# Kernel optimization log

Measured on AMD Instinct MI355X. Metric: run time of the kernel, lower is better.

## Reference

```python
import jax, jax.numpy as jnp
import numpy as np

MB, SEQ, EMBDIM, N_TOKENS = 8, 2048, 64, 8192


def setup_inputs() -> dict:
    key = jax.random.key(0)
    k1, k2 = jax.random.split(key)
    X = jax.random.normal(k1, (MB, SEQ, EMBDIM), dtype=jnp.float32)
    weight = jax.random.normal(k2, (N_TOKENS, EMBDIM), dtype=jnp.float32)
    return {"X": X, "weight": weight}


def reference(X, weight):
    adotb = jnp.einsum("bse,ne->bsn", X, weight)            # [mb, seq, n_tokens]
    adota = jnp.sum(X * X, axis=-1, keepdims=True)           # [mb, seq, 1]
    bdotb = jnp.sum(weight * weight, axis=-1)                # [n_tokens]
    dist = adota - 2.0 * adotb + bdotb                       # [mb, seq, n_tokens]
    return jnp.argmin(dist, axis=-1)                         # [mb, seq] int indices
```

## Files before the change

kernel.cpp:

```cpp
#include <hip/hip_runtime.h>
#include <math.h>

#define EMB     64
#define NTOK    8192
#define NQ      16384
#define TPB     256
#define CSPLIT  4
#define CRANGE  (NTOK / CSPLIT)
#define BQ      128
#define TILE_C  128
#define NT      (CRANGE / TILE_C)
#define TCH     (TILE_C * EMB)
#define NXBLK   (NQ / BQ)

typedef _Float16 half8 __attribute__((ext_vector_type(8)));
typedef float    f32x4 __attribute__((ext_vector_type(4)));

__device__ __forceinline__ void gl2lds16(const _Float16* g, _Float16* l) {
    __builtin_amdgcn_global_load_lds(
        (const __attribute__((address_space(1))) unsigned int*)g,
        (__attribute__((address_space(3))) unsigned int*)l, 16, 0, 0);
}

__device__ __forceinline__ unsigned long long pack_di(float d, int idx) {
    unsigned int u = __float_as_uint(d);
    unsigned int m = (u & 0x80000000u) ? ~u : (u | 0x80000000u);
    return ((unsigned long long)m << 32) | (unsigned int)idx;
}

__global__ void prep_kernel(const float* __restrict__ W,
                            _Float16* __restrict__ Wh, _Float16* __restrict__ Wl,
                            float* __restrict__ ynorm,
                            unsigned long long* __restrict__ packed,
                            int* __restrict__ cnt) {
    const int gtid = blockIdx.x * blockDim.x + threadIdx.x;
    if (gtid < NQ)    packed[gtid] = ~0ull;
    if (gtid < NXBLK) cnt[gtid] = 0;
    if (gtid < NTOK * 8) {
        const int u  = gtid;
        const int g  = u >> 7, rem = u & 127;
        const int kb = rem >> 6, ln = rem & 63;
        const int r  = ln & 15, lq = ln >> 4;
        const int c  = g * 16 + r;
        const float* wp = W + (size_t)c * EMB + kb * 32 + lq * 8;
        float4 v0 = *(const float4*)wp;
        float4 v1 = *(const float4*)(wp + 4);
        float xv[8] = {v0.x, v0.y, v0.z, v0.w, v1.x, v1.y, v1.z, v1.w};
        half8 h, l;
#pragma unroll
        for (int j = 0; j < 8; ++j) {
            _Float16 hh = (_Float16)xv[j];
            h[j] = hh;
            l[j] = (_Float16)(xv[j] - (float)hh);
        }
        *(half8*)(Wh + (size_t)u * 8) = h;
        *(half8*)(Wl + (size_t)u * 8) = l;
    } else if (gtid < NTOK * 8 + NTOK) {
        const int c = gtid - NTOK * 8;
        const float4* w4 = (const float4*)(W + (size_t)c * EMB);
        float s = 0.f;
#pragma unroll
        for (int i = 0; i < EMB / 4; ++i) {
            float4 v = w4[i];
            s = fmaf(v.x, v.x, s); s = fmaf(v.y, v.y, s);
            s = fmaf(v.z, v.z, s); s = fmaf(v.w, v.w, s);
        }
        ynorm[c] = s;
    }
}

__global__ __launch_bounds__(TPB, 2) void vq_mfma_kernel(
    const float* __restrict__ X,
    const _Float16* __restrict__ Wh, const _Float16* __restrict__ Wl,
    const float* __restrict__ ynorm,
    unsigned long long* __restrict__ packed,
    int* __restrict__ cnt, int* __restrict__ out)
{
    __shared__ __align__(16) _Float16 LdsH[3][TCH];
    __shared__ __align__(16) float    Lyn[CRANGE];
    __shared__ float RedV[2][BQ];
    __shared__ int   RedI[2][BQ];
    __shared__ int   fin;

    const int t    = threadIdx.x;
    const int lane = t & 63;
    const int wid  = t >> 6;
    const int wq   = wid & 1;
    const int wy   = wid >> 1;
    const int l15  = lane & 15;
    const int lq   = lane >> 4;

    const int bx     = blockIdx.x;
    const int qblk   = bx * BQ;
    const int qbase  = qblk + wq * 64;
    const int cbase0 = blockIdx.y * CRANGE;

#pragma unroll
    for (int pt = 0; pt < 2; ++pt) {
        const size_t gsbase = (size_t)(cbase0 + pt * TILE_C) * 64;
#pragma unroll
        for (int i = 0; i < 4; ++i) {
            const int jw = i * 256 + wid * 64;
            gl2lds16(Wh + gsbase + (size_t)(jw + lane) * 8, &LdsH[pt][0] + (size_t)jw * 8);
        }
    }

    for (int u = t; u < CRANGE / 4; u += TPB)
        ((float4*)Lyn)[u] = ((const float4*)(ynorm + cbase0))[u];

    half8 ah[4][2], al[4][2];
#pragma unroll
    for (int mt = 0; mt < 4; ++mt) {
#pragma unroll
        for (int kb = 0; kb < 2; ++kb) {
            const float* xp = X + (size_t)(qbase + mt * 16 + l15) * EMB + kb * 32 + lq * 8;
            float4 v0 = *(const float4*)xp;
            float4 v1 = *(const float4*)(xp + 4);
            float xv[8] = {v0.x, v0.y, v0.z, v0.w, v1.x, v1.y, v1.z, v1.w};
            half8 h, l;
#pragma unroll
            for (int j = 0; j < 8; ++j) {
                _Float16 hh = (_Float16)xv[j];
                h[j] = hh;
                l[j] = (_Float16)(xv[j] - (float)hh);
            }
            ah[mt][kb] = h;
            al[mt][kb] = l;
        }
    }

    float minv[4][4];
    int   mini[4][4];
#pragma unroll
    for (int mt = 0; mt < 4; ++mt)
#pragma unroll
        for (int r = 0; r < 4; ++r) { minv[mt][r] = INFINITY; mini[mt][r] = 0; }

    const f32x4 zero4 = {0.f, 0.f, 0.f, 0.f};

    __syncthreads();

    for (int tt = 0; tt < NT; ++tt) {
        const int cb = cbase0 + tt * TILE_C;

        half8 blr[4][2];
#pragma unroll
        for (int ct = 0; ct < 4; ++ct) {
            const size_t gc = (size_t)cb * 8 + (wy * 4 + ct) * 128 + lane;
            blr[ct][0] = *(const half8*)(Wl + gc * 8);
            blr[ct][1] = *(const half8*)(Wl + (gc + 64) * 8);
        }

        if (tt + 2 < NT) {
            const size_t gsbase = (size_t)(cb + 2 * TILE_C) * 64;
            _Float16* dst = &LdsH[(tt + 2) % 3][0];
#pragma unroll
            for (int i = 0; i < 4; ++i) {
                const int jw = i * 256 + wid * 64;
                gl2lds16(Wh + gsbase + (size_t)(jw + lane) * 8, dst + (size_t)jw * 8);
            }
        }

        const _Float16* LH = &LdsH[tt % 3][0];
        const int c0 = tt * TILE_C;
#pragma unroll
        for (int ct = 0; ct < 4; ++ct) {
            const int chunk0 = (wy * 4 + ct) * 128 + lane;
            half8 bh0 = *(const half8*)(LH + (size_t)chunk0 * 8);
            half8 bh1 = *(const half8*)(LH + (size_t)(chunk0 + 64) * 8);
            f32x4 acc[4];
#pragma unroll
            for (int mt = 0; mt < 4; ++mt) {
                f32x4 a = __builtin_amdgcn_mfma_f32_16x16x32_f16(al[mt][0], bh0, zero4, 0, 0, 0);
                a = __builtin_amdgcn_mfma_f32_16x16x32_f16(ah[mt][0], blr[ct][0], a, 0, 0, 0);
                a = __builtin_amdgcn_mfma_f32_16x16x32_f16(ah[mt][0], bh0, a, 0, 0, 0);
                a = __builtin_amdgcn_mfma_f32_16x16x32_f16(al[mt][1], bh1, a, 0, 0, 0);
                a = __builtin_amdgcn_mfma_f32_16x16x32_f16(ah[mt][1], blr[ct][1], a, 0, 0, 0);
                a = __builtin_amdgcn_mfma_f32_16x16x32_f16(ah[mt][1], bh1, a, 0, 0, 0);
                acc[mt] = a;
            }
            const int   ccol = wy * 64 + ct * 16;
            const float yn   = Lyn[c0 + ccol + l15];
            const int   cidx = cb + ccol + l15;
#pragma unroll
            for (int mt = 0; mt < 4; ++mt) {
#pragma unroll
                for (int r = 0; r < 4; ++r) {
                    float s = fmaf(-2.f, acc[mt][r], yn);
                    if (s < minv[mt][r]) { minv[mt][r] = s; mini[mt][r] = cidx; }
                }
            }
        }

        __builtin_amdgcn_s_barrier();
    }

#pragma unroll
    for (int mt = 0; mt < 4; ++mt) {
#pragma unroll
        for (int r = 0; r < 4; ++r) {
            float v = minv[mt][r];
            int   i = mini[mt][r];
#pragma unroll
            for (int m = 1; m <= 8; m <<= 1) {
                float ov = __shfl_xor(v, m, 64);
                int   oi = __shfl_xor(i, m, 64);
                if (ov < v || (ov == v && oi < i)) { v = ov; i = oi; }
            }
            if (l15 == 0) {
                int qoff = wq * 64 + mt * 16 + lq * 4 + r;
                RedV[wy][qoff] = v;
                RedI[wy][qoff] = i;
            }
        }
    }
    __syncthreads();

    if (t < BQ) {
        float v0 = RedV[0][t]; int i0 = RedI[0][t];
        float v1 = RedV[1][t]; int i1 = RedI[1][t];
        if (v1 < v0 || (v1 == v0 && i1 < i0)) { v0 = v1; i0 = i1; }
        atomicMin(&packed[qblk + t], pack_di(v0, i0));
    }
    asm volatile("s_waitcnt vmcnt(0)" ::: "memory");
    __syncthreads();
    if (t == 0) fin = (atomicAdd(&cnt[bx], 1) == CSPLIT - 1);
    __syncthreads();
    if (fin && t < BQ) {
        unsigned long long v = atomicMin(&packed[qblk + t], ~0ull);
        out[qblk + t] = (int)(unsigned int)(v & 0xFFFFFFFFu);
    }
}

extern "C" void kernel_launch(void* const* d_in, const int* in_sizes, int n_in,
                              void* d_out, int out_size, void* d_ws, size_t ws_size,
                              hipStream_t stream) {
    const float* X = (const float*)d_in[0];
    const float* W = (const float*)d_in[1];

    _Float16* Wh    = (_Float16*)d_ws;
    _Float16* Wl    = Wh + (size_t)NTOK * EMB;
    float*    ynorm = (float*)(Wl + (size_t)NTOK * EMB);
    unsigned long long* packed = (unsigned long long*)(ynorm + NTOK);
    int*      cnt   = (int*)(packed + NQ);
    int*      out   = (int*)d_out;

    prep_kernel<<<(NTOK * 8 + NTOK) / TPB, TPB, 0, stream>>>(W, Wh, Wl, ynorm, packed, cnt);
    dim3 grid(NXBLK, CSPLIT);
    vq_mfma_kernel<<<grid, TPB, 0, stream>>>(X, Wh, Wl, ynorm, packed, cnt, out);
}
```

Measured before the change: 116.7 us.

## Give each wave private double-buffered LDS staging and drop per-tile block barrier

Replaces the block-shared triple-buffered LDS tile of high-half weights with per-wave private double buffers, where each wave loads only the codebook chunk it consumes. Synchronisation moves from a block-wide s_barrier each tile to an explicit per-wave vmcnt wait, so waves can drift independently and overlap loads with MFMA work. In exchange, the two waves sharing a wy now load the same data separately, which doubles high-half traffic. Correctness also depends on the hand-counted vmcnt(8) value matching the number of loads the compiler actually keeps outstanding.

Result: no change. 117.1 us (+0.3%).

```diff
diff --git a/kernel.cpp b/kernel.cpp
--- a/kernel.cpp
+++ b/kernel.cpp
@@ -10,8 +10,8 @@
 #define BQ      128
 #define TILE_C  128
 #define NT      (CRANGE / TILE_C)
-#define TCH     (TILE_C * EMB)
 #define NXBLK   (NQ / BQ)
+#define WCH     512
 
 typedef _Float16 half8 __attribute__((ext_vector_type(8)));
 typedef float    f32x4 __attribute__((ext_vector_type(4)));
@@ -76,7 +76,7 @@
     unsigned long long* __restrict__ packed,
     int* __restrict__ cnt, int* __restrict__ out)
 {
-    __shared__ __align__(16) _Float16 LdsH[3][TCH];
+    __shared__ __align__(16) _Float16 LdsP[4][2][WCH * 8];
     __shared__ __align__(16) float    Lyn[CRANGE];
     __shared__ float RedV[2][BQ];
     __shared__ int   RedI[2][BQ];
@@ -95,14 +95,14 @@
     const int qbase  = qblk + wq * 64;
     const int cbase0 = blockIdx.y * CRANGE;
 
-#pragma unroll
-    for (int pt = 0; pt < 2; ++pt) {
-        const size_t gsbase = (size_t)(cbase0 + pt * TILE_C) * 64;
-#pragma unroll
-        for (int i = 0; i < 4; ++i) {
-            const int jw = i * 256 + wid * 64;
-            gl2lds16(Wh + gsbase + (size_t)(jw + lane) * 8, &LdsH[pt][0] + (size_t)jw * 8);
-        }
+    _Float16* const myP0 = &LdsP[wid][0][0];
+    _Float16* const myP1 = &LdsP[wid][1][0];
+
+    {
+        const size_t gch = (size_t)cbase0 * 8 + wy * WCH;
+#pragma unroll
+        for (int i = 0; i < 8; ++i)
+            gl2lds16(Wh + (gch + i * 64 + lane) * 8, myP0 + (size_t)i * 64 * 8);
     }
 
     for (int u = t; u < CRANGE / 4; u += TPB)
@@ -140,34 +140,35 @@
 
     __syncthreads();
 
+#pragma unroll 1
     for (int tt = 0; tt < NT; ++tt) {
-        const int cb = cbase0 + tt * TILE_C;
+        const int    cb  = cbase0 + tt * TILE_C;
+        const size_t gch = (size_t)cb * 8 + wy * WCH;
 
         half8 blr[4][2];
 #pragma unroll
         for (int ct = 0; ct < 4; ++ct) {
-            const size_t gc = (size_t)cb * 8 + (wy * 4 + ct) * 128 + lane;
-            blr[ct][0] = *(const half8*)(Wl + gc * 8);
-            blr[ct][1] = *(const half8*)(Wl + (gc + 64) * 8);
-        }
-
-        if (tt + 2 < NT) {
-            const size_t gsbase = (size_t)(cb + 2 * TILE_C) * 64;
-            _Float16* dst = &LdsH[(tt + 2) % 3][0];
-#pragma unroll
-            for (int i = 0; i < 4; ++i) {
-                const int jw = i * 256 + wid * 64;
-                gl2lds16(Wh + gsbase + (size_t)(jw + lane) * 8, dst + (size_t)jw * 8);
-            }
-        }
-
-        const _Float16* LH = &LdsH[tt % 3][0];
+            blr[ct][0] = *(const half8*)(Wl + (gch + ct * 128 + lane) * 8);
+            blr[ct][1] = *(const half8*)(Wl + (gch + ct * 128 + 64 + lane) * 8);
+        }
+
+        if (tt + 1 < NT) {
+            const size_t gnx = gch + TILE_C * 8;
+            _Float16* dst = (tt & 1) ? myP0 : myP1;
+#pragma unroll
+            for (int i = 0; i < 8; ++i)
+                gl2lds16(Wh + (gnx + i * 64 + lane) * 8, dst + (size_t)i * 64 * 8);
+        }
+
+        asm volatile("s_waitcnt vmcnt(8)" ::: "memory");
+        __builtin_amdgcn_sched_barrier(0);
+
+        const _Float16* LB = (tt & 1) ? myP1 : myP0;
         const int c0 = tt * TILE_C;
 #pragma unroll
         for (int ct = 0; ct < 4; ++ct) {
-            const int chunk0 = (wy * 4 + ct) * 128 + lane;
-            half8 bh0 = *(const half8*)(LH + (size_t)chunk0 * 8);
-            half8 bh1 = *(const half8*)(LH + (size_t)(chunk0 + 64) * 8);
+            half8 bh0 = *(const half8*)(LB + (size_t)(ct * 128 + lane) * 8);
+            half8 bh1 = *(const half8*)(LB + (size_t)(ct * 128 + 64 + lane) * 8);
             f32x4 acc[4];
 #pragma unroll
             for (int mt = 0; mt < 4; ++mt) {
@@ -191,8 +192,6 @@
                 }
             }
         }
-
-        __builtin_amdgcn_s_barrier();
     }
 
 #pragma unroll
```
